# Performance work log

Hardware: AMD Instinct MI355X
Metric: run time of the kernel (lower is better)

The kernel has to match this reference:

```python
import jax, jax.numpy as jnp
import numpy as np

V = 32000   # num_tokens
D = 1024    # dim
L = 4       # depth
H = 8       # heads
B = 2       # batch
T = 2048    # seq_len (divisible by H)
SCALE = (D // H) ** -0.5  # scale uses dim//heads as in source
EPS = 1e-5
NEG_SLOPE = 0.01  # LeakyReLU default


def layernorm(x, g, b):
    mu = jnp.mean(x, axis=-1, keepdims=True)
    var = jnp.mean(jnp.square(x - mu), axis=-1, keepdims=True)
    return (x - mu) * jax.lax.rsqrt(var + EPS) * g + b


def setup_inputs() -> dict:
    key = jax.random.key(0)
    ks = jax.random.split(key, 8)
    s = 0.02
    f = lambda k, shape: jax.random.normal(k, shape, jnp.float32) * s
    return {
        "x": jax.random.randint(ks[0], (B, T), 0, V),
        "token_emb": f(ks[1], (V, D)),
        "ln1_g": jnp.ones((L, D), jnp.float32), "ln1_b": jnp.zeros((L, D), jnp.float32),
        "wqkv": f(ks[2], (L, D, 3 * D)),
        "wout_w": f(ks[3], (L, D, D)), "wout_b": jnp.zeros((L, D), jnp.float32),
        "ln2_g": jnp.ones((L, D), jnp.float32), "ln2_b": jnp.zeros((L, D), jnp.float32),
        "ff1_w": f(ks[4], (L, D, 4 * D)), "ff1_b": jnp.zeros((L, 4 * D), jnp.float32),
        "ff2_w": f(ks[5], (L, 4 * D, D)), "ff2_b": jnp.zeros((L, D), jnp.float32),
        "logit_w": f(ks[6], (D, V)), "logit_b": jnp.zeros((V,), jnp.float32),
    }


def reference(x, token_emb, ln1_g, ln1_b, wqkv, wout_w, wout_b,
              ln2_g, ln2_b, ff1_w, ff1_b, ff2_w, ff2_b, logit_w, logit_b):
    h = token_emb[x]  # [B, T, D]
    for i in range(L):
        # --- Residual(PreNorm(SelfAttention)) ---
        y = layernorm(h, ln1_g[i], ln1_b[i])
        qkv = y @ wqkv[i]                      # [B, T, 3D]
        q, k, v = jnp.split(qkv, 3, axis=-1)
        # faithful to source: reshape(b, -1, h, e) with e = full dim -> heads
        # partition the sequence into H strided groups, head-dim = D
        rs = lambda t: t.reshape(B, T // H, H, D).transpose(0, 2, 1, 3)  # [B, H, T/H, D]
        q, k, v = rs(q), rs(k), rs(v)
        dots = jnp.einsum('bhid,bhjd->bhij', q, k) * SCALE
        attn = jax.nn.softmax(dots, axis=-1)
        o = jnp.einsum('bhij,bhjd->bhid', attn, v)
        o = o.transpose(0, 2, 1, 3).reshape(B, T, D)
        h = h + (o @ wout_w[i] + wout_b[i])
        # --- Residual(PreNorm(FeedForward)) ---
        y = layernorm(h, ln2_g[i], ln2_b[i])
        y = y @ ff1_w[i] + ff1_b[i]
        y = jnp.where(y >= 0, y, NEG_SLOPE * y)  # LeakyReLU
        h = h + (y @ ff2_w[i] + ff2_b[i])
    return h @ logit_w + logit_b  # [B, T, V]
```

## Files before the change

kernel.cpp:

```cpp
#include <hip/hip_runtime.h>

#define DD 1024
#define LL 4
#define HH 8
#define BB 2
#define TT 2048
#define VV 32000
#define SCALE_QK 0.08838834764831845f

typedef __bf16 bf16x8 __attribute__((ext_vector_type(8)));
typedef __bf16 bf16x4 __attribute__((ext_vector_type(4)));
typedef float  f32x4  __attribute__((ext_vector_type(4)));

__device__ __forceinline__ void gload_lds16(const void* g, void* l) {
  __builtin_amdgcn_global_load_lds((const __attribute__((address_space(1))) void*)g,
                                   (__attribute__((address_space(3))) void*)l, 16, 0, 0);
}

template<int MODE>
__global__ __launch_bounds__(256, 2)
void gemm_mt(const __bf16* __restrict__ A, long ldA, long aSB, long aSH,
             const __bf16* __restrict__ Bt, long ldB, long bSB, long bSH,
             void* __restrict__ Cv, long ldC, long cSB, long cSH,
             const float* __restrict__ bias,
             const float* __restrict__ res, long ldR,
             int K)
{
  extern __shared__ __attribute__((aligned(16))) char smem[];

  int zbh = blockIdx.z;
  if (MODE == 5) {
    const int kc = zbh >> 4;
    zbh &= 15;
    A  += (size_t)kc * K;
    Bt += (size_t)kc * K;
  }
  const int zb = zbh >> 3, zh = zbh & 7;
  A  += (size_t)zb * aSB + (size_t)zh * aSH;
  Bt += (size_t)zb * bSB + (size_t)zh * bSH;
  const size_t cOff = (size_t)zb * cSB + (size_t)zh * cSH;

  const int nbx = gridDim.x, nby = gridDim.y;
  const int nwg = nbx * nby;
  const int fid = blockIdx.y * nbx + blockIdx.x;
  const int q8 = nwg >> 3, r8 = nwg & 7;
  const int xcd = fid & 7, idx = fid >> 3;
  const int swz = (xcd < r8 ? xcd * (q8 + 1) : r8 * (q8 + 1) + (xcd - r8) * q8) + idx;
  int bx, by;
  if ((nby & 1) == 0) {
    const int W = 2 * nbx;
    const int grp = swz / W, t = swz - grp * W;
    bx = t >> 1; by = grp * 2 + (t & 1);
  } else {
    bx = swz / nby; by = swz - bx * nby;
  }
  const int m0 = by * 256, n0 = bx * 128;

  const int tid = threadIdx.x;
  const int wv = tid >> 6, ln = tid & 63;
  const int wm = wv >> 1, wn = wv & 1;

  const int usA = (ln & 7) ^ (ln >> 3);
  const int rsA = wv * 64 + 2 * (ln >> 3) + (usA >> 2);
  const int ksA = (usA & 3) * 8;
  const __bf16* pA0 = A + (size_t)(m0 + rsA) * ldA + ksA;
  const int usB = (tid & 7) ^ ((tid >> 3) & 7);
  const int rsB = 2 * (tid >> 3) + (usB >> 2);
  const int ksB = (usB & 3) * 8;
  const __bf16* pB0 = Bt + (size_t)(n0 + rsB) * ldB + ksB;

  const int lr = ln & 15;
  const int gfr = ((((ln & 1) << 2) | ((ln >> 4) & 3)) ^ ((ln >> 1) & 7)) << 4;
  const int aR = (wm * 64 + (lr >> 1)) * 128 + gfr;
  const int bR = 49152 + (wn * 32 + (lr >> 1)) * 128 + gfr;

  f32x4 acc[8][4] = {};
  const int NT = K >> 5;

#define STG(sl) { \
    char* da = smem + (sl) * 16384 + wv * 4096 + ln * 16; \
    gload_lds16(pA0,            da); \
    gload_lds16(pA0 + 16 * ldA, da + 1024); \
    gload_lds16(pA0 + 32 * ldA, da + 2048); \
    gload_lds16(pA0 + 48 * ldA, da + 3072); \
    char* db = smem + 49152 + (sl) * 8192 + tid * 16; \
    gload_lds16(pB0,            db); \
    gload_lds16(pB0 + 64 * ldB, db + 4096); \
    pA0 += 32; pB0 += 32; }

  STG(0);
  if (NT > 1) {
    STG(1);
    asm volatile("s_waitcnt vmcnt(6)" ::: "memory");
  } else {
    asm volatile("s_waitcnt vmcnt(0)" ::: "memory");
  }
  __builtin_amdgcn_s_barrier();

  int sc = 0, sn = 1, sf = 2;
  for (int t = 0; t < NT; ++t) {
    if (t + 2 < NT) STG(sf);
    const char* aBase = smem + sc * 16384 + aR;
    const char* bBase = smem + sc * 8192 + bR;
    bf16x8 a[8], b[4];
#pragma unroll
    for (int j = 0; j < 4; j++) b[j] = *(const bf16x8*)(bBase + j * 1024);
#pragma unroll
    for (int i = 0; i < 8; i++) a[i] = *(const bf16x8*)(aBase + i * 1024);
    __builtin_amdgcn_s_setprio(1);
#pragma unroll
    for (int i = 0; i < 8; i++)
#pragma unroll
      for (int j = 0; j < 4; j++)
        acc[i][j] = __builtin_amdgcn_mfma_f32_16x16x32_bf16(a[i], b[j], acc[i][j], 0, 0, 0);
    __builtin_amdgcn_s_setprio(0);
    if (t + 1 < NT) {
      if (t + 2 < NT) { asm volatile("s_waitcnt vmcnt(6)" ::: "memory"); }
      else            { asm volatile("s_waitcnt vmcnt(0)" ::: "memory"); }
      __builtin_amdgcn_sched_barrier(0);
      __builtin_amdgcn_s_barrier();
    }
    const int tmp = sc; sc = sn; sn = sf; sf = tmp;
  }
#undef STG

  const int rb = m0 + wm * 128 + (ln >> 4) * 4;
  const int cb = n0 + wn * 64 + lr;
#pragma unroll
  for (int i = 0; i < 8; i++)
#pragma unroll
    for (int j = 0; j < 4; j++) {
      const int col = cb + j * 16;
#pragma unroll
      for (int r = 0; r < 4; r++) {
        const int row = rb + i * 16 + r;
        float v = acc[i][j][r];
        const size_t ci = cOff + (size_t)row * ldC + col;
        if (MODE == 0)      ((__bf16*)Cv)[ci] = (__bf16)v;
        else if (MODE == 1) ((float*)Cv)[ci] = v;
        else if (MODE == 2) ((float*)Cv)[ci] = v + bias[col] + res[(size_t)row * ldR + col];
        else if (MODE == 3) { v += bias[col]; ((__bf16*)Cv)[ci] = (__bf16)(v >= 0.f ? v : 0.01f * v); }
        else if (MODE == 4) ((float*)Cv)[ci] = v + bias[col];
        else if (MODE == 5) atomicAdd(&((float*)Cv)[ci], v);
      }
    }
}

__global__ void wtrans(const float* __restrict__ W, __bf16* __restrict__ Wt, int K, int N)
{
  const size_t zo = (size_t)blockIdx.z * K * N;
  __shared__ float t[32][33];
  const int n0 = blockIdx.x * 32, k0 = blockIdx.y * 32;
  const int tx = threadIdx.x, ty = threadIdx.y;
#pragma unroll
  for (int r = 0; r < 4; r++)
    t[ty + r * 8][tx] = W[zo + (size_t)(k0 + ty + r * 8) * N + n0 + tx];
  __syncthreads();
#pragma unroll
  for (int r = 0; r < 4; r++)
    Wt[zo + (size_t)(n0 + ty + r * 8) * K + k0 + tx] = (__bf16)t[tx][ty + r * 8];
}

__global__ void vtrans(const __bf16* __restrict__ qkv, __bf16* __restrict__ Vt)
{
  const int z = blockIdx.z, bb = z >> 3, hh = z & 7;
  const __bf16* src = qkv + ((size_t)bb * TT + hh) * (3 * DD) + 2 * DD;
  __bf16* dst = Vt + (size_t)z * DD * 256;
  __shared__ __bf16 t[32][33];
  const int n0 = blockIdx.x * 32, i0 = blockIdx.y * 32;
  const int tx = threadIdx.x, ty = threadIdx.y;
#pragma unroll
  for (int r = 0; r < 4; r++)
    t[ty + r * 8][tx] = src[(size_t)(i0 + ty + r * 8) * (HH * 3 * DD) + n0 + tx];
  __syncthreads();
#pragma unroll
  for (int r = 0; r < 4; r++)
    dst[(size_t)(n0 + ty + r * 8) * 256 + i0 + tx] = t[tx][ty + r * 8];
}

__global__ void embed_k(const int* __restrict__ x, const float* __restrict__ emb, float* __restrict__ h)
{
  const int row = blockIdx.x;
  const int tok = x[row];
  ((float4*)(h + (size_t)row * DD))[threadIdx.x] = ((const float4*)(emb + (size_t)tok * DD))[threadIdx.x];
}

__global__ void ln_rows(const float* __restrict__ x, const float* __restrict__ g,
                        const float* __restrict__ b, __bf16* __restrict__ y)
{
  const int row = blockIdx.x, t = threadIdx.x;
  const int wv = t >> 6, ln = t & 63;
  const float4 v = ((const float4*)(x + (size_t)row * DD))[t];
  float s  = v.x + v.y + v.z + v.w;
  float ss = v.x * v.x + v.y * v.y + v.z * v.z + v.w * v.w;
#pragma unroll
  for (int o = 32; o; o >>= 1) { s += __shfl_xor(s, o); ss += __shfl_xor(ss, o); }
  __shared__ float rs_[4], rss_[4];
  if (!ln) { rs_[wv] = s; rss_[wv] = ss; }
  __syncthreads();
  s  = rs_[0] + rs_[1] + rs_[2] + rs_[3];
  ss = rss_[0] + rss_[1] + rss_[2] + rss_[3];
  const float mu  = s * (1.0f / DD);
  const float var = ss * (1.0f / DD) - mu * mu;
  const float r   = rsqrtf(var + 1e-5f);
  const float4 gv = ((const float4*)g)[t];
  const float4 bv = ((const float4*)b)[t];
  bf16x4 o = { (__bf16)((v.x - mu) * r * gv.x + bv.x),
               (__bf16)((v.y - mu) * r * gv.y + bv.y),
               (__bf16)((v.z - mu) * r * gv.z + bv.z),
               (__bf16)((v.w - mu) * r * gv.w + bv.w) };
  ((bf16x4*)(y + (size_t)row * DD))[t] = o;
}

__global__ void softmax256(const float* __restrict__ S, __bf16* __restrict__ P)
{
  const int row = blockIdx.x, t = threadIdx.x;
  const int wv = t >> 6, ln = t & 63;
  const float v = S[(size_t)row * 256 + t] * SCALE_QK;
  float m = v;
#pragma unroll
  for (int o = 32; o; o >>= 1) m = fmaxf(m, __shfl_xor(m, o));
  __shared__ float red[8];
  if (!ln) red[wv] = m;
  __syncthreads();
  m = fmaxf(fmaxf(red[0], red[1]), fmaxf(red[2], red[3]));
  const float e = __expf(v - m);
  float s = e;
#pragma unroll
  for (int o = 32; o; o >>= 1) s += __shfl_xor(s, o);
  if (!ln) red[4 + wv] = s;
  __syncthreads();
  s = red[4] + red[5] + red[6] + red[7];
  P[(size_t)row * 256 + t] = (__bf16)(e / s);
}

__global__ void f2bf(const float* __restrict__ h, __bf16* __restrict__ y)
{
  const size_t i = (size_t)blockIdx.x * 256 + threadIdx.x;
  const float4 a = ((const float4*)h)[2 * i];
  const float4 b = ((const float4*)h)[2 * i + 1];
  bf16x8 o = { (__bf16)a.x, (__bf16)a.y, (__bf16)a.z, (__bf16)a.w,
               (__bf16)b.x, (__bf16)b.y, (__bf16)b.z, (__bf16)b.w };
  ((bf16x8*)y)[i] = o;
}

template<int MODE>
static void G(const __bf16* A, long ldA, long aSB, long aSH,
              const __bf16* Bt, long ldB, long bSB, long bSH,
              void* C, long ldC, long cSB, long cSH,
              const float* bias, const float* res, long ldR,
              int M, int N, int K, int Z, hipStream_t s)
{
  hipFuncSetAttribute((const void*)gemm_mt<MODE>,
                      hipFuncAttributeMaxDynamicSharedMemorySize, 73728);
  gemm_mt<MODE><<<dim3(N / 128, M / 256, Z), 256, 73728, s>>>(
      A, ldA, aSB, aSH, Bt, ldB, bSB, bSH, C, ldC, cSB, cSH, bias, res, ldR, K);
}

extern "C" void kernel_launch(void* const* d_in, const int* in_sizes, int n_in,
                              void* d_out, int out_size, void* d_ws, size_t ws_size,
                              hipStream_t stream)
{
  const int*   x       = (const int*)  d_in[0];
  const float* emb     = (const float*)d_in[1];
  const float* ln1_g   = (const float*)d_in[2];
  const float* ln1_b   = (const float*)d_in[3];
  const float* wqkv    = (const float*)d_in[4];
  const float* wout_w  = (const float*)d_in[5];
  const float* wout_b  = (const float*)d_in[6];
  const float* ln2_g   = (const float*)d_in[7];
  const float* ln2_b   = (const float*)d_in[8];
  const float* ff1_w   = (const float*)d_in[9];
  const float* ff1_b   = (const float*)d_in[10];
  const float* ff2_w   = (const float*)d_in[11];
  const float* ff2_b   = (const float*)d_in[12];
  const float* logit_w = (const float*)d_in[13];
  const float* logit_b = (const float*)d_in[14];
  float* out = (float*)d_out;

  char* w = (char*)d_ws;
  size_t off = 0;
  auto take = [&](size_t bytes) { void* p = w + off; off += (bytes + 255) & ~(size_t)255; return p; };
  __bf16* wqkvT = (__bf16*)take((size_t)LL * 3 * DD * DD * 2);
  __bf16* woutT = (__bf16*)take((size_t)LL * DD * DD * 2);
  __bf16* ff1T  = (__bf16*)take((size_t)LL * 4 * DD * DD * 2);
  __bf16* ff2T  = (__bf16*)take((size_t)LL * DD * 4 * DD * 2);
  __bf16* logT  = (__bf16*)take((size_t)VV * DD * 2);
  float*  h     = (float*) take((size_t)BB * TT * DD * 4);
  __bf16* ybf   = (__bf16*)take((size_t)BB * TT * DD * 2);
  __bf16* qkvbf = (__bf16*)take((size_t)BB * TT * 3 * DD * 2);
  float*  Smat  = (float*) take((size_t)BB * HH * 256 * 256 * 4);
  __bf16* Pbf   = (__bf16*)take((size_t)BB * HH * 256 * 256 * 2);
  __bf16* Vt    = (__bf16*)take((size_t)BB * HH * DD * 256 * 2);
  __bf16* Obf   = (__bf16*)take((size_t)BB * TT * DD * 2);
  __bf16* midbf = (__bf16*)take((size_t)BB * TT * 4 * DD * 2);
  if (ws_size < off) return;

  const dim3 tb(32, 8);
  wtrans<<<dim3(3 * DD / 32, DD / 32, LL), tb, 0, stream>>>(wqkv,   wqkvT, DD, 3 * DD);
  wtrans<<<dim3(DD / 32,     DD / 32, LL), tb, 0, stream>>>(wout_w, woutT, DD, DD);
  wtrans<<<dim3(4 * DD / 32, DD / 32, LL), tb, 0, stream>>>(ff1_w,  ff1T,  DD, 4 * DD);
  wtrans<<<dim3(DD / 32, 4 * DD / 32, LL), tb, 0, stream>>>(ff2_w,  ff2T,  4 * DD, DD);
  wtrans<<<dim3(VV / 32,     DD / 32, 1),  tb, 0, stream>>>(logit_w, logT, DD, VV);

  const int M = BB * TT;
  embed_k<<<M, 256, 0, stream>>>(x, emb, h);

  for (int l = 0; l < LL; l++) {
    ln_rows<<<M, 256, 0, stream>>>(h, ln1_g + l * DD, ln1_b + l * DD, ybf);
    G<0>(ybf, DD, 0, 0, wqkvT + (size_t)l * 3 * DD * DD, DD, 0, 0,
         qkvbf, 3 * DD, 0, 0, nullptr, nullptr, 0, M, 3 * DD, DD, 1, stream);
    hipMemsetAsync(Smat, 0, (size_t)BB * HH * 256 * 256 * 4, stream);
    G<5>(qkvbf, HH * 3 * DD, (long)TT * 3 * DD, 3 * DD,
         qkvbf + DD, HH * 3 * DD, (long)TT * 3 * DD, 3 * DD,
         Smat, 256, (long)HH * 256 * 256, 256 * 256,
         nullptr, nullptr, 0, 256, 256, DD / 4, 4 * BB * HH, stream);
    softmax256<<<BB * HH * 256, 256, 0, stream>>>(Smat, Pbf);
    vtrans<<<dim3(DD / 32, 256 / 32, BB * HH), tb, 0, stream>>>(qkvbf, Vt);
    G<0>(Pbf, 256, (long)HH * 256 * 256, 256 * 256,
         Vt, 256, (long)HH * DD * 256, (long)DD * 256,
         Obf, HH * DD, (long)TT * DD, DD,
         nullptr, nullptr, 0, 256, DD, 256, BB * HH, stream);
    G<2>(Obf, DD, 0, 0, woutT + (size_t)l * DD * DD, DD, 0, 0,
         h, DD, 0, 0, wout_b + l * DD, h, DD, M, DD, DD, 1, stream);
    ln_rows<<<M, 256, 0, stream>>>(h, ln2_g + l * DD, ln2_b + l * DD, ybf);
    G<3>(ybf, DD, 0, 0, ff1T + (size_t)l * 4 * DD * DD, DD, 0, 0,
         midbf, 4 * DD, 0, 0, ff1_b + (size_t)l * 4 * DD, nullptr, 0, M, 4 * DD, DD, 1, stream);
    G<2>(midbf, 4 * DD, 0, 0, ff2T + (size_t)l * DD * 4 * DD, 4 * DD, 0, 0,
         h, DD, 0, 0, ff2_b + l * DD, h, DD, M, DD, 4 * DD, 1, stream);
  }

  f2bf<<<(M * DD / 8) / 256, 256, 0, stream>>>(h, ybf);
  G<4>(ybf, DD, 0, 0, logT, DD, 0, 0,
       out, VV, 0, 0, logit_b, nullptr, 0, M, VV, DD, 1, stream);
}
```

Before: 1.383 ms.

## Split-K the FF2 GEMM into four partials and fold reduction into layernorm

The FF2 GEMM (K=4096, N=1024) is now split into four K-chunks launched along the z dimension. Each chunk writes a separate fp32 partial buffer, which gives four times as many workgroups on a GEMM that otherwise fills few CUs. The partials, the ff2 bias and the residual are summed in the next layer's first layernorm kernel, or in a new final f2bf kernel, so no extra reduction launch is needed. The cost is 64MB of extra partial writes and reads per layer plus a larger workspace.

New measurement: 1.301 ms (median of 2 runs). 1.06x faster.

```diff
diff --git a/kernel.cpp b/kernel.cpp
--- a/kernel.cpp
+++ b/kernel.cpp
@@ -29,16 +29,18 @@
   extern __shared__ __attribute__((aligned(16))) char smem[];
 
   int zbh = blockIdx.z;
-  if (MODE == 5) {
-    const int kc = zbh >> 4;
-    zbh &= 15;
+  int kc = 0;
+  if (MODE == 5) { kc = zbh >> 4; zbh &= 15; }
+  if (MODE == 7) { kc = zbh; zbh = 0; }
+  if (MODE == 5 || MODE == 7) {
     A  += (size_t)kc * K;
     Bt += (size_t)kc * K;
   }
   const int zb = zbh >> 3, zh = zbh & 7;
   A  += (size_t)zb * aSB + (size_t)zh * aSH;
   Bt += (size_t)zb * bSB + (size_t)zh * bSH;
-  const size_t cOff = (size_t)zb * cSB + (size_t)zh * cSH;
+  const size_t cOff = (MODE == 7) ? (size_t)kc * cSB
+                                  : (size_t)zb * cSB + (size_t)zh * cSH;
 
   const int nbx = gridDim.x, nby = gridDim.y;
   const int nwg = nbx * nby;
@@ -142,6 +144,7 @@
         else if (MODE == 3) { v += bias[col]; ((__bf16*)Cv)[ci] = (__bf16)(v >= 0.f ? v : 0.01f * v); }
         else if (MODE == 4) ((float*)Cv)[ci] = v + bias[col];
         else if (MODE == 5) atomicAdd(&((float*)Cv)[ci], v);
+        else if (MODE == 7) ((float*)Cv)[ci] = v;
       }
     }
 }
@@ -212,6 +215,59 @@
   ((bf16x4*)(y + (size_t)row * DD))[t] = o;
 }
 
+__global__ void ln_acc(float* __restrict__ h, const float* __restrict__ P, long pStride,
+                       const float* __restrict__ bias2,
+                       const float* __restrict__ g, const float* __restrict__ b,
+                       __bf16* __restrict__ y)
+{
+  const int row = blockIdx.x, t = threadIdx.x;
+  const int wv = t >> 6, ln = t & 63;
+  float4 v = ((const float4*)(h + (size_t)row * DD))[t];
+#pragma unroll
+  for (int c = 0; c < 4; c++) {
+    const float4 p = ((const float4*)(P + (size_t)c * pStride + (size_t)row * DD))[t];
+    v.x += p.x; v.y += p.y; v.z += p.z; v.w += p.w;
+  }
+  const float4 b2 = ((const float4*)bias2)[t];
+  v.x += b2.x; v.y += b2.y; v.z += b2.z; v.w += b2.w;
+  ((float4*)(h + (size_t)row * DD))[t] = v;
+  float s  = v.x + v.y + v.z + v.w;
+  float ss = v.x * v.x + v.y * v.y + v.z * v.z + v.w * v.w;
+#pragma unroll
+  for (int o = 32; o; o >>= 1) { s += __shfl_xor(s, o); ss += __shfl_xor(ss, o); }
+  __shared__ float rs_[4], rss_[4];
+  if (!ln) { rs_[wv] = s; rss_[wv] = ss; }
+  __syncthreads();
+  s  = rs_[0] + rs_[1] + rs_[2] + rs_[3];
+  ss = rss_[0] + rss_[1] + rss_[2] + rss_[3];
+  const float mu  = s * (1.0f / DD);
+  const float var = ss * (1.0f / DD) - mu * mu;
+  const float r   = rsqrtf(var + 1e-5f);
+  const float4 gv = ((const float4*)g)[t];
+  const float4 bv = ((const float4*)b)[t];
+  bf16x4 o = { (__bf16)((v.x - mu) * r * gv.x + bv.x),
+               (__bf16)((v.y - mu) * r * gv.y + bv.y),
+               (__bf16)((v.z - mu) * r * gv.z + bv.z),
+               (__bf16)((v.w - mu) * r * gv.w + bv.w) };
+  ((bf16x4*)(y + (size_t)row * DD))[t] = o;
+}
+
+__global__ void f2bf_acc(const float* __restrict__ h, const float* __restrict__ P, long pStride,
+                         const float* __restrict__ bias2, __bf16* __restrict__ y)
+{
+  const int row = blockIdx.x, t = threadIdx.x;
+  float4 v = ((const float4*)(h + (size_t)row * DD))[t];
+#pragma unroll
+  for (int c = 0; c < 4; c++) {
+    const float4 p = ((const float4*)(P + (size_t)c * pStride + (size_t)row * DD))[t];
+    v.x += p.x; v.y += p.y; v.z += p.z; v.w += p.w;
+  }
+  const float4 b2 = ((const float4*)bias2)[t];
+  bf16x4 o = { (__bf16)(v.x + b2.x), (__bf16)(v.y + b2.y),
+               (__bf16)(v.z + b2.z), (__bf16)(v.w + b2.w) };
+  ((bf16x4*)(y + (size_t)row * DD))[t] = o;
+}
+
 __global__ void softmax256(const float* __restrict__ S, __bf16* __restrict__ P)
 {
   const int row = blockIdx.x, t = threadIdx.x;
@@ -232,16 +288,6 @@
   __syncthreads();
   s = red[4] + red[5] + red[6] + red[7];
   P[(size_t)row * 256 + t] = (__bf16)(e / s);
-}
-
-__global__ void f2bf(const float* __restrict__ h, __bf16* __restrict__ y)
-{
-  const size_t i = (size_t)blockIdx.x * 256 + threadIdx.x;
-  const float4 a = ((const float4*)h)[2 * i];
-  const float4 b = ((const float4*)h)[2 * i + 1];
-  bf16x8 o = { (__bf16)a.x, (__bf16)a.y, (__bf16)a.z, (__bf16)a.w,
-               (__bf16)b.x, (__bf16)b.y, (__bf16)b.z, (__bf16)b.w };
-  ((bf16x8*)y)[i] = o;
 }
 
 template<int MODE>
@@ -278,6 +324,8 @@
   const float* logit_b = (const float*)d_in[14];
   float* out = (float*)d_out;
 
+  const int M = BB * TT;
+
   char* w = (char*)d_ws;
   size_t off = 0;
   auto take = [&](size_t bytes) { void* p = w + off; off += (bytes + 255) & ~(size_t)255; return p; };
@@ -286,14 +334,15 @@
   __bf16* ff1T  = (__bf16*)take((size_t)LL * 4 * DD * DD * 2);
   __bf16* ff2T  = (__bf16*)take((size_t)LL * DD * 4 * DD * 2);
   __bf16* logT  = (__bf16*)take((size_t)VV * DD * 2);
-  float*  h     = (float*) take((size_t)BB * TT * DD * 4);
-  __bf16* ybf   = (__bf16*)take((size_t)BB * TT * DD * 2);
-  __bf16* qkvbf = (__bf16*)take((size_t)BB * TT * 3 * DD * 2);
+  float*  h     = (float*) take((size_t)M * DD * 4);
+  __bf16* ybf   = (__bf16*)take((size_t)M * DD * 2);
+  __bf16* qkvbf = (__bf16*)take((size_t)M * 3 * DD * 2);
   float*  Smat  = (float*) take((size_t)BB * HH * 256 * 256 * 4);
   __bf16* Pbf   = (__bf16*)take((size_t)BB * HH * 256 * 256 * 2);
   __bf16* Vt    = (__bf16*)take((size_t)BB * HH * DD * 256 * 2);
-  __bf16* Obf   = (__bf16*)take((size_t)BB * TT * DD * 2);
-  __bf16* midbf = (__bf16*)take((size_t)BB * TT * 4 * DD * 2);
+  __bf16* Obf   = (__bf16*)take((size_t)M * DD * 2);
+  __bf16* midbf = (__bf16*)take((size_t)M * 4 * DD * 2);
+  float*  part  = (float*) take((size_t)4 * M * DD * 4);
   if (ws_size < off) return;
 
   const dim3 tb(32, 8);
@@ -303,11 +352,14 @@
   wtrans<<<dim3(DD / 32, 4 * DD / 32, LL), tb, 0, stream>>>(ff2_w,  ff2T,  4 * DD, DD);
   wtrans<<<dim3(VV / 32,     DD / 32, 1),  tb, 0, stream>>>(logit_w, logT, DD, VV);
 
-  const int M = BB * TT;
   embed_k<<<M, 256, 0, stream>>>(x, emb, h);
 
   for (int l = 0; l < LL; l++) {
-    ln_rows<<<M, 256, 0, stream>>>(h, ln1_g + l * DD, ln1_b + l * DD, ybf);
+    if (l == 0)
+      ln_rows<<<M, 256, 0, stream>>>(h, ln1_g, ln1_b, ybf);
+    else
+      ln_acc<<<M, 256, 0, stream>>>(h, part, (long)M * DD, ff2_b + (size_t)(l - 1) * DD,
+                                    ln1_g + (size_t)l * DD, ln1_b + (size_t)l * DD, ybf);
     G<0>(ybf, DD, 0, 0, wqkvT + (size_t)l * 3 * DD * DD, DD, 0, 0,
          qkvbf, 3 * DD, 0, 0, nullptr, nullptr, 0, M, 3 * DD, DD, 1, stream);
     hipMemsetAsync(Smat, 0, (size_t)BB * HH * 256 * 256 * 4, stream);
@@ -322,15 +374,15 @@
          Obf, HH * DD, (long)TT * DD, DD,
          nullptr, nullptr, 0, 256, DD, 256, BB * HH, stream);
     G<2>(Obf, DD, 0, 0, woutT + (size_t)l * DD * DD, DD, 0, 0,
-         h, DD, 0, 0, wout_b + l * DD, h, DD, M, DD, DD, 1, stream);
-    ln_rows<<<M, 256, 0, stream>>>(h, ln2_g + l * DD, ln2_b + l * DD, ybf);
+         h, DD, 0, 0, wout_b + (size_t)l * DD, h, DD, M, DD, DD, 1, stream);
+    ln_rows<<<M, 256, 0, stream>>>(h, ln2_g + (size_t)l * DD, ln2_b + (size_t)l * DD, ybf);
     G<3>(ybf, DD, 0, 0, ff1T + (size_t)l * 4 * DD * DD, DD, 0, 0,
          midbf, 4 * DD, 0, 0, ff1_b + (size_t)l * 4 * DD, nullptr, 0, M, 4 * DD, DD, 1, stream);
-    G<2>(midbf, 4 * DD, 0, 0, ff2T + (size_t)l * DD * 4 * DD, 4 * DD, 0, 0,
-         h, DD, 0, 0, ff2_b + l * DD, h, DD, M, DD, 4 * DD, 1, stream);
-  }
-
-  f2bf<<<(M * DD / 8) / 256, 256, 0, stream>>>(h, ybf);
+    G<7>(midbf, 4 * DD, 0, 0, ff2T + (size_t)l * DD * 4 * DD, 4 * DD, 0, 0,
+         part, DD, (long)M * DD, 0, nullptr, nullptr, 0, M, DD, DD, 4, stream);
+  }
+
+  f2bf_acc<<<M, 256, 0, stream>>>(h, part, (long)M * DD, ff2_b + (size_t)3 * DD, ybf);
   G<4>(ybf, DD, 0, 0, logT, DD, 0, 0,
        out, VV, 0, 0, logit_b, nullptr, 0, M, VV, DD, 1, stream);
 }
```
